# Kernel tuning notes

Measured on AMD Instinct MI355X. Metric: run time of the kernel, lower is better.

## Reference

```python
import jax, jax.numpy as jnp
import numpy as np

DIM = 1024
HEADS = 16
HEAD_DIM = 64
INNER = HEADS * HEAD_DIM


def setup_inputs() -> dict:
    key = jax.random.key(0)
    ks = jax.random.split(key, 6)
    x = jax.random.normal(ks[0], (4, 2048, DIM), dtype=jnp.float32)
    # torch nn.Linear weight shape [out, in]; store as [in, out] for x @ W
    Wq = jax.random.normal(ks[1], (DIM, INNER), dtype=jnp.float32) * (DIM ** -0.5)
    Wk = jax.random.normal(ks[2], (DIM, INNER), dtype=jnp.float32) * (DIM ** -0.5)
    Wv = jax.random.normal(ks[3], (DIM, INNER), dtype=jnp.float32) * (DIM ** -0.5)
    Wo = jax.random.normal(ks[4], (INNER, DIM), dtype=jnp.float32) * (INNER ** -0.5)
    bo = jax.random.normal(ks[5], (DIM,), dtype=jnp.float32) * 0.01
    return {"x": x, "Wq": Wq, "Wk": Wk, "Wv": Wv, "Wo": Wo, "bo": bo}


def reference(x, Wq, Wk, Wv, Wo, bo):
    b, n, _ = x.shape
    # projections, split heads: [b, n, inner] -> [b, h, n, d]
    split = lambda t: t.reshape(b, n, HEADS, HEAD_DIM).transpose(0, 2, 1, 3)
    q = split(x @ Wq)
    k = split(x @ Wk)
    v = split(x @ Wv)
    scale = HEAD_DIM ** -0.5
    sim = jnp.einsum('bhnd,bhmd->bhnm', q, k) * scale
    attn = jax.nn.softmax(sim, axis=-1)
    out = jnp.einsum('bhnm,bhmd->bhnd', attn, v)
    out = out.transpose(0, 2, 1, 3).reshape(b, n, INNER)
    return out @ Wo + bo
```

## Files before the change

### kernel.cpp

```cpp
#include <hip/hip_runtime.h>
#include <hip/hip_bf16.h>
#include <stdint.h>

typedef unsigned short u16;
typedef __bf16 bf16x8_t __attribute__((ext_vector_type(8)));
typedef float f32x4_t __attribute__((ext_vector_type(4)));
typedef float f32x16_t __attribute__((ext_vector_type(16)));
typedef unsigned int u32x2_t __attribute__((ext_vector_type(2)));

__device__ __forceinline__ u16 f2bf(float f) {
    union { float f; uint32_t u; } c; c.f = f;
    uint32_t r = c.u + 0x7FFFu + ((c.u >> 16) & 1u);
    return (u16)(r >> 16);
}

__device__ __forceinline__ uint32_t pk2(float a, float b) {
    union { __bf16 h[2]; uint32_t u; } z;
    z.h[0] = (__bf16)a; z.h[1] = (__bf16)b;
    return z.u;
}

__device__ __forceinline__ void gld_lds16(const void* g, void* l) {
    __builtin_amdgcn_global_load_lds(
        (__attribute__((address_space(1))) void*)(g),
        (__attribute__((address_space(3))) void*)(l), 16, 0, 0);
}

#define QSCALE 0.18033688011112042f

__global__ void k_convert_x(const float* __restrict__ x, u16* __restrict__ xb) {
    int i = blockIdx.x * 256 + threadIdx.x;
    float4 v = ((const float4*)x)[i];
    ushort4 o;
    o.x = f2bf(v.x); o.y = f2bf(v.y); o.z = f2bf(v.z); o.w = f2bf(v.w);
    ((ushort4*)xb)[i] = o;
}

__global__ void k_convert_wT(const float* __restrict__ w0, const float* __restrict__ w1,
                             const float* __restrict__ w2, const float* __restrict__ w3,
                             u16* __restrict__ wT) {
    __shared__ u16 t[32][33];
    const float* src = (blockIdx.z == 0) ? w0 : (blockIdx.z == 1) ? w1 : (blockIdx.z == 2) ? w2 : w3;
    u16* dst = wT + (size_t)blockIdx.z * (1024 * 1024);
    int n0 = blockIdx.x * 32, k0 = blockIdx.y * 32;
    int tx = threadIdx.x & 31, ty = threadIdx.x >> 5;
    #pragma unroll
    for (int r = 0; r < 4; ++r) {
        int kl = ty * 4 + r;
        t[tx][kl] = f2bf(src[(size_t)(k0 + kl) * 1024 + n0 + tx]);
    }
    __syncthreads();
    #pragma unroll
    for (int r = 0; r < 4; ++r) {
        int nl = ty * 4 + r;
        dst[(size_t)(n0 + nl) * 1024 + k0 + tx] = t[nl][tx];
    }
}

template <int MODE>
__global__ __launch_bounds__(256, 2) void k_gemm(
    const u16* __restrict__ A, const u16* __restrict__ WT,
    const float* __restrict__ bias,
    u16* __restrict__ qo, u16* __restrict__ ko, u16* __restrict__ vt,
    float* __restrict__ out) {
    __shared__ u16 lA[128 * 32];
    __shared__ u16 lB[128 * 32];
    const int tid = threadIdx.x, wv = tid >> 6, ln = tid & 63;
    const int lo = ln & 15, jg = ln >> 4;
    const int m0 = blockIdx.x * 128;
    int mat, n0;
    if (MODE == 0) { mat = blockIdx.y >> 3; n0 = (blockIdx.y & 7) * 128; }
    else           { mat = 3;               n0 = blockIdx.y * 128; }
    const u16* Bt = WT + (size_t)mat * (1024 * 1024);
    const int wm = wv >> 1, wn = wv & 1;

    f32x4_t acc[4][4];
    #pragma unroll
    for (int i = 0; i < 4; ++i)
        #pragma unroll
        for (int j = 0; j < 4; ++j) acc[i][j] = (f32x4_t){0.f, 0.f, 0.f, 0.f};

    for (int k0 = 0; k0 < 1024; k0 += 32) {
        __syncthreads();
        #pragma unroll
        for (int is = 0; is < 2; ++is) {
            int c = is * 256 + tid;
            int r = c >> 2;
            int j = (c & 3) ^ ((r >> 1) & 3);
            gld_lds16(A  + (size_t)(m0 + r) * 1024 + k0 + j * 8, &lA[(is * 256 + wv * 64) * 8]);
            gld_lds16(Bt + (size_t)(n0 + r) * 1024 + k0 + j * 8, &lB[(is * 256 + wv * 64) * 8]);
        }
        __syncthreads();
        bf16x8_t af[4], bfr[4];
        #pragma unroll
        for (int i = 0; i < 4; ++i) {
            int r = wm * 64 + i * 16 + lo;
            af[i] = *(const bf16x8_t*)&lA[(r * 4 + (jg ^ ((r >> 1) & 3))) * 8];
        }
        #pragma unroll
        for (int j = 0; j < 4; ++j) {
            int r = wn * 64 + j * 16 + lo;
            bfr[j] = *(const bf16x8_t*)&lB[(r * 4 + (jg ^ ((r >> 1) & 3))) * 8];
        }
        #pragma unroll
        for (int i = 0; i < 4; ++i)
            #pragma unroll
            for (int j = 0; j < 4; ++j)
                acc[i][j] = __builtin_amdgcn_mfma_f32_16x16x32_bf16(af[i], bfr[j], acc[i][j], 0, 0, 0);
    }

    if (MODE == 0) {
        if (mat == 2) {
            #pragma unroll
            for (int j = 0; j < 4; ++j) {
                int col = n0 + wn * 64 + j * 16 + lo;
                int hh = col >> 6, dd = col & 63;
                #pragma unroll
                for (int i = 0; i < 4; ++i) {
                    int m = m0 + wm * 64 + i * 16 + jg * 4;
                    int bb = m >> 11, nn = m & 2047;
                    ushort4 pkv;
                    pkv.x = f2bf(acc[i][j][0]);
                    pkv.y = f2bf(acc[i][j][1]);
                    pkv.z = f2bf(acc[i][j][2]);
                    pkv.w = f2bf(acc[i][j][3]);
                    *(ushort4*)&vt[(((size_t)(bb * 16 + hh)) * 64 + dd) * 2048 + nn] = pkv;
                }
            }
        } else {
            u16* dst = (mat == 0) ? qo : ko;
            float sc = (mat == 0) ? QSCALE : 1.0f;
            #pragma unroll
            for (int j = 0; j < 4; ++j) {
                int col = n0 + wn * 64 + j * 16 + lo;
                int hh = col >> 6, dd = col & 63;
                #pragma unroll
                for (int i = 0; i < 4; ++i)
                    #pragma unroll
                    for (int rg = 0; rg < 4; ++rg) {
                        int m = m0 + wm * 64 + i * 16 + jg * 4 + rg;
                        int bb = m >> 11, nn = m & 2047;
                        dst[(((size_t)(bb * 16 + hh)) * 2048 + nn) * 64 + dd] = f2bf(acc[i][j][rg] * sc);
                    }
            }
        }
    } else {
        #pragma unroll
        for (int j = 0; j < 4; ++j) {
            int col = n0 + wn * 64 + j * 16 + lo;
            float bv = bias[col];
            #pragma unroll
            for (int i = 0; i < 4; ++i)
                #pragma unroll
                for (int rg = 0; rg < 4; ++rg) {
                    int m = m0 + wm * 64 + i * 16 + jg * 4 + rg;
                    out[(size_t)m * 1024 + col] = acc[i][j][rg] + bv;
                }
        }
    }
}

__global__ __launch_bounds__(256, 4) void k_attn(
    const u16* __restrict__ Q, const u16* __restrict__ K,
    const u16* __restrict__ Vg, u16* __restrict__ ctx) {
    __shared__ __align__(16) u16 Kl[2][64 * 64];
    __shared__ __align__(16) u16 Vt[2][64 * 64];

    const int tid = threadIdx.x, wv = tid >> 6, ln = tid & 63;
    const int lq = ln & 31, hi = ln >> 5;
    const int bh = blockIdx.x;
    const int b = bh >> 4, h = bh & 15;
    const size_t base = (size_t)bh * 2048 * 64;
    const u16* Vtg = Vg + (size_t)bh * 64 * 2048;
    const int q0 = blockIdx.y * 128 + wv * 32;

    bf16x8_t bQ[4];
    {
        const u16* qp = Q + base + (size_t)(q0 + lq) * 64 + hi * 8;
        #pragma unroll
        for (int s = 0; s < 4; ++s) bQ[s] = *(const bf16x8_t*)(qp + s * 16);
    }
    bf16x8_t ones;
    #pragma unroll
    for (int e = 0; e < 8; ++e) ones[e] = (__bf16)1.0f;

    f32x16_t acc[2], lacc;
    #pragma unroll
    for (int e = 0; e < 16; ++e) { acc[0][e] = 0.f; acc[1][e] = 0.f; lacc[e] = 0.f; }

    auto stageK = [&](int buf, int kv0) {
        #pragma unroll
        for (int is = 0; is < 2; ++is) {
            int c = is * 256 + tid;
            int r = c >> 3;
            int j = (c & 7) ^ (r & 7);
            gld_lds16(K + base + (size_t)(kv0 + r) * 64 + j * 8,
                      &Kl[buf][(is * 256 + wv * 64) * 8]);
        }
    };
    auto stageV = [&](int buf, int kv0) {
        #pragma unroll
        for (int is = 0; is < 2; ++is) {
            int c = is * 256 + tid;
            int r = c >> 3;
            int j = (c & 7) ^ (r & 7);
            gld_lds16(Vtg + (size_t)r * 2048 + kv0 + j * 8,
                      &Vt[buf][(is * 256 + wv * 64) * 8]);
        }
    };

    stageK(0, 0);
    stageV(0, 0);
    __syncthreads();

    const int swl = lq & 7;

    for (int t = 0; t < 32; ++t) {
        const int c = t & 1;
        if (t < 31) {
            stageK(c ^ 1, (t + 1) * 64);
            stageV(c ^ 1, (t + 1) * 64);
        }

        #pragma unroll
        for (int kg = 0; kg < 2; ++kg) {
            f32x16_t z;
            #pragma unroll
            for (int e = 0; e < 16; ++e) z[e] = 0.f;
            __builtin_amdgcn_s_setprio(1);
            #pragma unroll
            for (int s = 0; s < 4; ++s) {
                const bf16x8_t aK = *(const bf16x8_t*)
                    &Kl[c][(kg * 32 + lq) * 64 + (((2 * s + hi) ^ swl) * 8)];
                z = __builtin_amdgcn_mfma_f32_32x32x16_bf16(aK, bQ[s], z, 0, 0, 0);
            }
            __builtin_amdgcn_s_setprio(0);
            uint32_t w[4][2];
            #pragma unroll
            for (int m = 0; m < 4; ++m) {
                float p0 = __builtin_amdgcn_exp2f(z[4 * m + 0]);
                float p1 = __builtin_amdgcn_exp2f(z[4 * m + 1]);
                float p2 = __builtin_amdgcn_exp2f(z[4 * m + 2]);
                float p3 = __builtin_amdgcn_exp2f(z[4 * m + 3]);
                w[m][0] = pk2(p0, p1);
                w[m][1] = pk2(p2, p3);
            }
            __builtin_amdgcn_s_setprio(1);
            #pragma unroll
            for (int sl = 0; sl < 2; ++sl) {
                const int ma = 2 * sl, sp = 2 * kg + sl;
                u32x2_t r0 = __builtin_amdgcn_permlane32_swap(w[ma][0], w[ma + 1][0], false, false);
                u32x2_t r1 = __builtin_amdgcn_permlane32_swap(w[ma][1], w[ma + 1][1], false, false);
                union { uint32_t u[4]; bf16x8_t v; } ap;
                ap.u[0] = r0[0]; ap.u[1] = r1[0]; ap.u[2] = r0[1]; ap.u[3] = r1[1];
                lacc = __builtin_amdgcn_mfma_f32_32x32x16_bf16(ap.v, ones, lacc, 0, 0, 0);
                #pragma unroll
                for (int dh = 0; dh < 2; ++dh) {
                    const bf16x8_t bV = *(const bf16x8_t*)
                        &Vt[c][(dh * 32 + lq) * 64 + (((2 * sp + hi) ^ swl) * 8)];
                    acc[dh] = __builtin_amdgcn_mfma_f32_32x32x16_bf16(ap.v, bV, acc[dh], 0, 0, 0);
                }
            }
            __builtin_amdgcn_s_setprio(0);
        }

        __syncthreads();
    }

    f32x16_t linv;
    #pragma unroll
    for (int e = 0; e < 16; ++e) linv[e] = 1.0f / lacc[e];
    #pragma unroll
    for (int dh = 0; dh < 2; ++dh) {
        int d = dh * 32 + lq;
        #pragma unroll
        for (int e = 0; e < 16; ++e) {
            int q = q0 + (e & 3) + 8 * (e >> 2) + 4 * hi;
            ctx[((size_t)(b * 2048 + q)) * 1024 + h * 64 + d] = f2bf(acc[dh][e] * linv[e]);
        }
    }
}

extern "C" void kernel_launch(void* const* d_in, const int* in_sizes, int n_in,
                              void* d_out, int out_size, void* d_ws, size_t ws_size,
                              hipStream_t stream) {
    const float* x  = (const float*)d_in[0];
    const float* Wq = (const float*)d_in[1];
    const float* Wk = (const float*)d_in[2];
    const float* Wv = (const float*)d_in[3];
    const float* Wo = (const float*)d_in[4];
    const float* bo = (const float*)d_in[5];
    float* out = (float*)d_out;

    char* ws = (char*)d_ws;
    u16* xb   = (u16*)(ws);
    u16* wT   = (u16*)(ws + 16777216);
    u16* qb   = (u16*)(ws + 25165824);
    u16* kb   = (u16*)(ws + 41943040);
    u16* vtb  = (u16*)(ws + 58720256);
    u16* ctx  = (u16*)(ws + 75497472);

    k_convert_x<<<8192, 256, 0, stream>>>(x, xb);
    k_convert_wT<<<dim3(32, 32, 4), 256, 0, stream>>>(Wq, Wk, Wv, Wo, wT);
    k_gemm<0><<<dim3(64, 24), 256, 0, stream>>>(xb, wT, nullptr, qb, kb, vtb, nullptr);
    k_attn<<<dim3(64, 16), 256, 0, stream>>>(qb, kb, vtb, ctx);
    k_gemm<1><<<dim3(64, 8), 256, 0, stream>>>(ctx, wT, bo, nullptr, nullptr, nullptr, out);
}
```

Baseline: 195.8 us.

## Deepen GEMM K-tile to 64 and run attention with 512-thread blocks

The GEMM main loop now stages a 64-wide K slice per iteration, using a new 8-chunk XOR swizzle and two MFMA sub-steps, which halves the number of barrier/stage rounds. The attention kernel moves to 512 threads covering 256 queries per block, so each K/V tile in LDS is shared by twice as many waves and each thread issues one staging load instead of two. The first QK MFMA also takes a constant zero accumulator instead of zeroing z on every step. The costs are double the LDS per GEMM block, which may lower occupancy, and fewer, larger attention blocks.

New measurement: 171.2 us. 12.6% less time.

```diff
diff --git a/kernel.cpp b/kernel.cpp
--- a/kernel.cpp
+++ b/kernel.cpp
@@ -63,8 +63,8 @@
     const float* __restrict__ bias,
     u16* __restrict__ qo, u16* __restrict__ ko, u16* __restrict__ vt,
     float* __restrict__ out) {
-    __shared__ u16 lA[128 * 32];
-    __shared__ u16 lB[128 * 32];
+    __shared__ u16 lA[128 * 64];
+    __shared__ u16 lB[128 * 64];
     const int tid = threadIdx.x, wv = tid >> 6, ln = tid & 63;
     const int lo = ln & 15, jg = ln >> 4;
     const int m0 = blockIdx.x * 128;
@@ -80,33 +80,36 @@
         #pragma unroll
         for (int j = 0; j < 4; ++j) acc[i][j] = (f32x4_t){0.f, 0.f, 0.f, 0.f};
 
-    for (int k0 = 0; k0 < 1024; k0 += 32) {
+    for (int k0 = 0; k0 < 1024; k0 += 64) {
         __syncthreads();
         #pragma unroll
-        for (int is = 0; is < 2; ++is) {
+        for (int is = 0; is < 4; ++is) {
             int c = is * 256 + tid;
-            int r = c >> 2;
-            int j = (c & 3) ^ ((r >> 1) & 3);
+            int r = c >> 3;
+            int j = (c & 7) ^ (r & 7);
             gld_lds16(A  + (size_t)(m0 + r) * 1024 + k0 + j * 8, &lA[(is * 256 + wv * 64) * 8]);
             gld_lds16(Bt + (size_t)(n0 + r) * 1024 + k0 + j * 8, &lB[(is * 256 + wv * 64) * 8]);
         }
         __syncthreads();
-        bf16x8_t af[4], bfr[4];
-        #pragma unroll
-        for (int i = 0; i < 4; ++i) {
-            int r = wm * 64 + i * 16 + lo;
-            af[i] = *(const bf16x8_t*)&lA[(r * 4 + (jg ^ ((r >> 1) & 3))) * 8];
-        }
-        #pragma unroll
-        for (int j = 0; j < 4; ++j) {
-            int r = wn * 64 + j * 16 + lo;
-            bfr[j] = *(const bf16x8_t*)&lB[(r * 4 + (jg ^ ((r >> 1) & 3))) * 8];
-        }
-        #pragma unroll
-        for (int i = 0; i < 4; ++i)
-            #pragma unroll
-            for (int j = 0; j < 4; ++j)
-                acc[i][j] = __builtin_amdgcn_mfma_f32_16x16x32_bf16(af[i], bfr[j], acc[i][j], 0, 0, 0);
+        #pragma unroll
+        for (int sub = 0; sub < 2; ++sub) {
+            bf16x8_t af[4], bfr[4];
+            #pragma unroll
+            for (int i = 0; i < 4; ++i) {
+                int r = wm * 64 + i * 16 + lo;
+                af[i] = *(const bf16x8_t*)&lA[(r * 8 + ((sub * 4 + jg) ^ (r & 7))) * 8];
+            }
+            #pragma unroll
+            for (int j = 0; j < 4; ++j) {
+                int r = wn * 64 + j * 16 + lo;
+                bfr[j] = *(const bf16x8_t*)&lB[(r * 8 + ((sub * 4 + jg) ^ (r & 7))) * 8];
+            }
+            #pragma unroll
+            for (int i = 0; i < 4; ++i)
+                #pragma unroll
+                for (int j = 0; j < 4; ++j)
+                    acc[i][j] = __builtin_amdgcn_mfma_f32_16x16x32_bf16(af[i], bfr[j], acc[i][j], 0, 0, 0);
+        }
     }
 
     if (MODE == 0) {
@@ -160,7 +163,7 @@
     }
 }
 
-__global__ __launch_bounds__(256, 4) void k_attn(
+__global__ __launch_bounds__(512, 4) void k_attn(
     const u16* __restrict__ Q, const u16* __restrict__ K,
     const u16* __restrict__ Vg, u16* __restrict__ ctx) {
     __shared__ __align__(16) u16 Kl[2][64 * 64];
@@ -172,7 +175,7 @@
     const int b = bh >> 4, h = bh & 15;
     const size_t base = (size_t)bh * 2048 * 64;
     const u16* Vtg = Vg + (size_t)bh * 64 * 2048;
-    const int q0 = blockIdx.y * 128 + wv * 32;
+    const int q0 = blockIdx.y * 256 + wv * 32;
 
     bf16x8_t bQ[4];
     {
@@ -183,30 +186,23 @@
     bf16x8_t ones;
     #pragma unroll
     for (int e = 0; e < 8; ++e) ones[e] = (__bf16)1.0f;
+    f32x16_t zro;
+    #pragma unroll
+    for (int e = 0; e < 16; ++e) zro[e] = 0.f;
 
     f32x16_t acc[2], lacc;
     #pragma unroll
     for (int e = 0; e < 16; ++e) { acc[0][e] = 0.f; acc[1][e] = 0.f; lacc[e] = 0.f; }
 
     auto stageK = [&](int buf, int kv0) {
-        #pragma unroll
-        for (int is = 0; is < 2; ++is) {
-            int c = is * 256 + tid;
-            int r = c >> 3;
-            int j = (c & 7) ^ (r & 7);
-            gld_lds16(K + base + (size_t)(kv0 + r) * 64 + j * 8,
-                      &Kl[buf][(is * 256 + wv * 64) * 8]);
-        }
+        int r = tid >> 3;
+        int j = (tid & 7) ^ (r & 7);
+        gld_lds16(K + base + (size_t)(kv0 + r) * 64 + j * 8, &Kl[buf][wv * 64 * 8]);
     };
     auto stageV = [&](int buf, int kv0) {
-        #pragma unroll
-        for (int is = 0; is < 2; ++is) {
-            int c = is * 256 + tid;
-            int r = c >> 3;
-            int j = (c & 7) ^ (r & 7);
-            gld_lds16(Vtg + (size_t)r * 2048 + kv0 + j * 8,
-                      &Vt[buf][(is * 256 + wv * 64) * 8]);
-        }
+        int r = tid >> 3;
+        int j = (tid & 7) ^ (r & 7);
+        gld_lds16(Vtg + (size_t)r * 2048 + kv0 + j * 8, &Vt[buf][wv * 64 * 8]);
     };
 
     stageK(0, 0);
@@ -225,11 +221,14 @@
         #pragma unroll
         for (int kg = 0; kg < 2; ++kg) {
             f32x16_t z;
-            #pragma unroll
-            for (int e = 0; e < 16; ++e) z[e] = 0.f;
             __builtin_amdgcn_s_setprio(1);
-            #pragma unroll
-            for (int s = 0; s < 4; ++s) {
+            {
+                const bf16x8_t aK = *(const bf16x8_t*)
+                    &Kl[c][(kg * 32 + lq) * 64 + ((hi ^ swl) * 8)];
+                z = __builtin_amdgcn_mfma_f32_32x32x16_bf16(aK, bQ[0], zro, 0, 0, 0);
+            }
+            #pragma unroll
+            for (int s = 1; s < 4; ++s) {
                 const bf16x8_t aK = *(const bf16x8_t*)
                     &Kl[c][(kg * 32 + lq) * 64 + (((2 * s + hi) ^ swl) * 8)];
                 z = __builtin_amdgcn_mfma_f32_32x32x16_bf16(aK, bQ[s], z, 0, 0, 0);
@@ -303,6 +302,6 @@
     k_convert_x<<<8192, 256, 0, stream>>>(x, xb);
     k_convert_wT<<<dim3(32, 32, 4), 256, 0, stream>>>(Wq, Wk, Wv, Wo, wT);
     k_gemm<0><<<dim3(64, 24), 256, 0, stream>>>(xb, wT, nullptr, qb, kb, vtb, nullptr);
-    k_attn<<<dim3(64, 16), 256, 0, stream>>>(qb, kb, vtb, ctx);
+    k_attn<<<dim3(64, 8), 512, 0, stream>>>(qb, kb, vtb, ctx);
     k_gemm<1><<<dim3(64, 8), 256, 0, stream>>>(ctx, wT, bo, nullptr, nullptr, nullptr, out);
 }
```
